# Kernel optimization log

Hardware: AMD Instinct MI355X
Metric: run time of the kernel (lower is better)

## Reference

```python
import jax, jax.numpy as jnp
import numpy as np

N = 200_000   # points
C = 20        # semantic classes
P = 256       # proposals (from bfs_cluster)
M = 400_000   # (proposal, point) pairs
CLUSTER_PROPOSE_POINTS = 100
VOXEL_SIZE = 0.02


def setup_inputs() -> dict:
    key = jax.random.key(0)
    k1, k2, k3, k4, k5 = jax.random.split(key, 5)
    return {
        "logit_pred": jax.random.normal(k1, (N, C), jnp.float32),
        "bias_pred": jax.random.normal(k2, (N, 3), jnp.float32),
        "coord": jax.random.normal(k3, (N, 3), jnp.float32) * 5.0,
        "proposal_ids": jax.random.randint(k4, (M,), 0, P, dtype=jnp.int32),
        "point_ids": jax.random.randint(k5, (M,), 0, N, dtype=jnp.int32),
    }


def reference(logit_pred, bias_pred, coord, proposal_ids, point_ids):
    # voxelized predicted instance centers (center_pred /= voxel_size)
    center_pred = (coord + bias_pred) / VOXEL_SIZE

    # softmax + argmax semantic prediction
    probs = jax.nn.softmax(logit_pred, axis=-1)          # [N, C]
    segment_pred = jnp.argmax(probs, axis=1)             # [N]

    # dense proposal mask construction (scatter): proposals_pred[pid, point] = 1
    proposals_pred = jnp.zeros((P, N), jnp.int32).at[proposal_ids, point_ids].set(1)
    counts = proposals_pred.sum(axis=1)                  # [P]
    proposals_mask = counts > CLUSTER_PROPOSE_POINTS     # [P] keep mask

    # instance class = semantic class of the representative (first) point per proposal
    rep = jax.ops.segment_min(point_ids, proposal_ids, num_segments=P)  # [P]
    instance_pred = segment_pred[jnp.clip(rep, 0, N - 1)]               # [P]

    # per-proposal mean confidence: mean over proposal points of probs[point, cls]
    conf = probs[:, instance_pred]                       # [N, P] gather of class columns
    score_sum = jnp.einsum("pn,np->p", proposals_pred.astype(probs.dtype), conf)
    pred_scores = jnp.where(proposals_mask,
                            score_sum / jnp.maximum(counts, 1).astype(probs.dtype),
                            0.0)                         # [P]

    # filtered masks/classes (kept at fixed shape; invalid rows zeroed / class -1)
    pred_masks = proposals_pred * proposals_mask[:, None].astype(jnp.int32)
    pred_classes = jnp.where(proposals_mask, instance_pred, -1)

    return pred_scores, pred_masks, pred_classes, bias_pred, probs
```

## Files before the change

kernel.cpp:

```cpp
#include <hip/hip_runtime.h>

static constexpr int    kN = 200000;
static constexpr int    kC = 20;
static constexpr int    kP = 256;
static constexpr int    kM = 400000;
static constexpr int    kThreshPts = 100;
static constexpr int    kRowCap = 2048;
static constexpr int    kLWords = kN / 32;
static constexpr int    kF4Total = kN * kC / 4;

typedef float nfloat4 __attribute__((ext_vector_type(4)));

static constexpr size_t OFF_SCORES  = 0;
static constexpr size_t OFF_MASKS   = 256;
static constexpr size_t OFF_CLASSES = OFF_MASKS + (size_t)kP * kN;
static constexpr size_t OFF_BIAS    = OFF_CLASSES + 256;
static constexpr size_t OFF_PROBS   = OFF_BIAS + 3 * (size_t)kN;

static constexpr size_t WS_CURSOR = 0;
static constexpr size_t WS_SEG    = 1024;
static constexpr size_t WS_ROWBUF = WS_SEG + (size_t)kN * 4;

__global__ void __launch_bounds__(256)
k_softmax(const float* __restrict__ logit,
          const float* __restrict__ bias,
          float* __restrict__ out,
          int* __restrict__ seg,
          int* __restrict__ cursor) {
    __shared__ float lds[256][21];
    int t = threadIdx.x;
    int gbase = blockIdx.x * 1280;

#pragma unroll
    for (int i = 0; i < 5; i++) {
        int g = gbase + i * 256 + t;
        if (g < kF4Total) {
            float4 v4 = ((const float4*)logit)[g];
            int lf = (g - gbase) * 4;
            float vv[4] = {v4.x, v4.y, v4.z, v4.w};
#pragma unroll
            for (int k = 0; k < 4; k++) {
                int fl = lf + k;
                lds[fl / kC][fl % kC] = vv[k];
            }
        }
    }
    if (blockIdx.x == 0) cursor[t] = 0;
    int tid = blockIdx.x * 256 + t;
    if (tid < 150000) {
        ((float4*)(out + OFF_BIAS))[tid] = ((const float4*)bias)[tid];
    }
    __syncthreads();

    bool valid = tid < kN;
    float v[kC];
    if (valid) {
#pragma unroll
        for (int i = 0; i < kC; i++) v[i] = lds[t][i];
        float m = v[0]; int arg = 0;
#pragma unroll
        for (int i = 1; i < kC; i++) if (v[i] > m) { m = v[i]; arg = i; }
        float ssum = 0.0f;
#pragma unroll
        for (int i = 0; i < kC; i++) { v[i] = __expf(v[i] - m); ssum += v[i]; }
        float inv = 1.0f / ssum;
#pragma unroll
        for (int i = 0; i < kC; i++) v[i] *= inv;
        seg[tid] = arg;
    }
    __syncthreads();
    if (valid) {
#pragma unroll
        for (int i = 0; i < kC; i++) lds[t][i] = v[i];
    }
    __syncthreads();

    float* probs = out + OFF_PROBS;
#pragma unroll
    for (int i = 0; i < 5; i++) {
        int g = gbase + i * 256 + t;
        if (g < kF4Total) {
            int lf = (g - gbase) * 4;
            float4 o;
            o.x = lds[(lf    ) / kC][(lf    ) % kC];
            o.y = lds[(lf + 1) / kC][(lf + 1) % kC];
            o.z = lds[(lf + 2) / kC][(lf + 2) % kC];
            o.w = lds[(lf + 3) / kC][(lf + 3) % kC];
            ((float4*)probs)[g] = o;
        }
    }
}

__global__ void k_bucket(const int* __restrict__ prop,
                         const int* __restrict__ pt,
                         int* __restrict__ cursor,
                         int* __restrict__ rowbuf) {
    __shared__ int s_cnt[kP];
    __shared__ int s_off[kP];
    int t = threadIdx.x;
    if (t < kP) s_cnt[t] = 0;
    __syncthreads();
    int base = blockIdx.x * 4096;
    int pv[4], nv[4], slot[4];
    bool val[4];
#pragma unroll
    for (int j = 0; j < 4; j++) {
        int idx = base + j * 1024 + t;
        val[j] = idx < kM;
        if (val[j]) {
            pv[j]   = prop[idx];
            nv[j]   = pt[idx];
            slot[j] = atomicAdd(&s_cnt[pv[j]], 1);
        }
    }
    __syncthreads();
    if (t < kP) s_off[t] = s_cnt[t] ? atomicAdd(&cursor[t], s_cnt[t]) : 0;
    __syncthreads();
#pragma unroll
    for (int j = 0; j < 4; j++) {
        if (val[j]) {
            int dst = s_off[pv[j]] + slot[j];
            if (dst < kRowCap) rowbuf[pv[j] * kRowCap + dst] = nv[j];
        }
    }
}

__global__ void __launch_bounds__(1024)
k_row(const int* __restrict__ rowbuf,
      const int* __restrict__ cursor,
      const int* __restrict__ seg,
      float* __restrict__ out) {
    __shared__ unsigned int lbits[kLWords];
    __shared__ int   s_redc[16];
    __shared__ int   s_redm[16];
    __shared__ float s_redf[16];
    __shared__ int   s_cls;
    __shared__ float s_fv;

    int p = blockIdx.x;
    int t = threadIdx.x;
    const float* probs = out + OFF_PROBS;

    for (int i = t; i < kLWords; i += 1024) lbits[i] = 0;
    int len = cursor[p];
    if (len > kRowCap) len = kRowCap;
    __syncthreads();

    int mymin = 0x7fffffff;
    const int* rb = rowbuf + p * kRowCap;
    for (int i = t; i < len; i += 1024) {
        int n = rb[i];
        atomicOr(&lbits[(unsigned)n >> 5], 1u << (n & 31));
        mymin = n < mymin ? n : mymin;
    }
    __syncthreads();

    int cnt = 0;
    for (int i = t; i < kLWords; i += 1024) cnt += __popc(lbits[i]);
    for (int off = 32; off; off >>= 1) {
        cnt += __shfl_down(cnt, off);
        int om = __shfl_down(mymin, off);
        mymin = om < mymin ? om : mymin;
    }
    if ((t & 63) == 0) { s_redc[t >> 6] = cnt; s_redm[t >> 6] = mymin; }
    __syncthreads();
    if (t == 0) {
        int tot = 0, mn = 0x7fffffff;
        for (int i = 0; i < 16; i++) {
            tot += s_redc[i];
            mn = s_redm[i] < mn ? s_redm[i] : mn;
        }
        int r = mn < 0 ? 0 : (mn > kN - 1 ? kN - 1 : mn);
        int c = seg[r];
        bool fl = tot > kThreshPts;
        s_cls = c;
        s_fv  = fl ? 1.0f : 0.0f;
        s_redc[0] = tot;
        out[OFF_CLASSES + p] = fl ? (float)c : -1.0f;
    }
    __syncthreads();
    int   tot = s_redc[0];
    float fv  = s_fv;
    int   c   = s_cls;

    float s = 0.0f;
    for (int i = t; i < len; i += 1024) {
        int n = rb[i];
        unsigned int bit = 1u << (n & 31);
        unsigned int old = atomicAnd(&lbits[(unsigned)n >> 5], ~bit);
        if (old & bit) s += probs[(size_t)n * kC + c];
    }
    for (int off = 32; off; off >>= 1) s += __shfl_down(s, off);
    if ((t & 63) == 0) s_redf[t >> 6] = s;
    __syncthreads();
    if (t == 0) {
        float stot = 0.0f;
        for (int i = 0; i < 16; i++) stot += s_redf[i];
        float denom = (float)(tot > 1 ? tot : 1);
        out[OFF_SCORES + p] = (fv != 0.0f) ? stot / denom : 0.0f;
    }

    for (int i = t; i < len; i += 1024) {
        int n = rb[i];
        atomicOr(&lbits[(unsigned)n >> 5], 1u << (n & 31));
    }
    __syncthreads();

    nfloat4* mrow = (nfloat4*)(out + OFF_MASKS) + (size_t)p * (kN / 4);
    for (int f = t; f < kN / 4; f += 1024) {
        unsigned int word = lbits[f >> 3];
        unsigned int b    = (word >> (((unsigned)f & 7u) * 4u)) & 0xFu;
        nfloat4 o;
        o.x = (b & 1u) ? fv : 0.0f;
        o.y = (b & 2u) ? fv : 0.0f;
        o.z = (b & 4u) ? fv : 0.0f;
        o.w = (b & 8u) ? fv : 0.0f;
        __builtin_nontemporal_store(o, &mrow[f]);
    }
}

extern "C" void kernel_launch(void* const* d_in, const int* in_sizes, int n_in,
                              void* d_out, int out_size, void* d_ws, size_t ws_size,
                              hipStream_t stream) {
    const float* logit = (const float*)d_in[0];
    const float* bias  = (const float*)d_in[1];
    const int* prop = (const int*)d_in[3];
    const int* pt   = (const int*)d_in[4];
    float* out = (float*)d_out;
    char*  ws  = (char*)d_ws;

    int* cursor = (int*)(ws + WS_CURSOR);
    int* seg    = (int*)(ws + WS_SEG);
    int* rowbuf = (int*)(ws + WS_ROWBUF);

    k_softmax<<<(kN + 255) / 256, 256, 0, stream>>>(logit, bias, out, seg, cursor);
    k_bucket<<<(kM + 4095) / 4096, 1024, 0, stream>>>(prop, pt, cursor, rowbuf);
    k_row<<<kP, 1024, 0, stream>>>(rowbuf, cursor, seg, out);
}
```

Before: 264.9 us.

## Split mask expansion into separate wide kernel reading global bitsets

Per-proposal bitsets built in LDS are now written to a global workspace. A new kernel with 4096 blocks of 256 threads expands them into the dense float mask output, replacing the loop inside the 256-block row kernel. Nontemporal stores become plain stores. The aim is to spread the roughly 200 MB mask write across many more blocks and waves than 256 large LDS-heavy blocks allow. The cost is an extra launch and a small global bitset round trip.

Result: no change. 266.3 us (+0.5%).

```diff
diff --git a/kernel.cpp b/kernel.cpp
--- a/kernel.cpp
+++ b/kernel.cpp
@@ -8,8 +8,8 @@
 static constexpr int    kRowCap = 2048;
 static constexpr int    kLWords = kN / 32;
 static constexpr int    kF4Total = kN * kC / 4;
-
-typedef float nfloat4 __attribute__((ext_vector_type(4)));
+static constexpr int    kSlices = 16;
+static constexpr int    kF4PerSlice = kN / 4 / kSlices;
 
 static constexpr size_t OFF_SCORES  = 0;
 static constexpr size_t OFF_MASKS   = 256;
@@ -18,8 +18,10 @@
 static constexpr size_t OFF_PROBS   = OFF_BIAS + 3 * (size_t)kN;
 
 static constexpr size_t WS_CURSOR = 0;
-static constexpr size_t WS_SEG    = 1024;
+static constexpr size_t WS_ROWVAL = 1024;
+static constexpr size_t WS_SEG    = 2048;
 static constexpr size_t WS_ROWBUF = WS_SEG + (size_t)kN * 4;
+static constexpr size_t WS_GBITS  = WS_ROWBUF + (size_t)kP * kRowCap * 4;
 
 __global__ void __launch_bounds__(256)
 k_softmax(const float* __restrict__ logit,
@@ -126,10 +128,12 @@
 }
 
 __global__ void __launch_bounds__(1024)
-k_row(const int* __restrict__ rowbuf,
-      const int* __restrict__ cursor,
-      const int* __restrict__ seg,
-      float* __restrict__ out) {
+k_meta(const int* __restrict__ rowbuf,
+       const int* __restrict__ cursor,
+       const int* __restrict__ seg,
+       unsigned int* __restrict__ gbits,
+       float* __restrict__ rowval,
+       float* __restrict__ out) {
     __shared__ unsigned int lbits[kLWords];
     __shared__ int   s_redc[16];
     __shared__ int   s_redm[16];
@@ -176,6 +180,7 @@
         s_cls = c;
         s_fv  = fl ? 1.0f : 0.0f;
         s_redc[0] = tot;
+        rowval[p] = fl ? 1.0f : 0.0f;
         out[OFF_CLASSES + p] = fl ? (float)c : -1.0f;
     }
     __syncthreads();
@@ -206,16 +211,30 @@
     }
     __syncthreads();
 
-    nfloat4* mrow = (nfloat4*)(out + OFF_MASKS) + (size_t)p * (kN / 4);
-    for (int f = t; f < kN / 4; f += 1024) {
-        unsigned int word = lbits[f >> 3];
+    unsigned int* grow = gbits + (size_t)p * kLWords;
+    for (int i = t; i < kLWords; i += 1024) grow[i] = lbits[i];
+}
+
+__global__ void __launch_bounds__(256)
+k_expand(const unsigned int* __restrict__ gbits,
+         const float* __restrict__ rowval,
+         float* __restrict__ masks) {
+    int p = blockIdx.x >> 4;
+    int q = blockIdx.x & 15;
+    float fv = rowval[p];
+    const unsigned int* row = gbits + (size_t)p * kLWords;
+    float4* mrow = (float4*)masks + (size_t)p * (kN / 4);
+    int fbase = q * kF4PerSlice;
+    int fend  = fbase + kF4PerSlice;
+    for (int f = fbase + threadIdx.x; f < fend; f += 256) {
+        unsigned int word = row[f >> 3];
         unsigned int b    = (word >> (((unsigned)f & 7u) * 4u)) & 0xFu;
-        nfloat4 o;
+        float4 o;
         o.x = (b & 1u) ? fv : 0.0f;
         o.y = (b & 2u) ? fv : 0.0f;
         o.z = (b & 4u) ? fv : 0.0f;
         o.w = (b & 8u) ? fv : 0.0f;
-        __builtin_nontemporal_store(o, &mrow[f]);
+        mrow[f] = o;
     }
 }
 
@@ -229,11 +248,14 @@
     float* out = (float*)d_out;
     char*  ws  = (char*)d_ws;
 
-    int* cursor = (int*)(ws + WS_CURSOR);
-    int* seg    = (int*)(ws + WS_SEG);
-    int* rowbuf = (int*)(ws + WS_ROWBUF);
+    int*          cursor = (int*)(ws + WS_CURSOR);
+    float*        rowval = (float*)(ws + WS_ROWVAL);
+    int*          seg    = (int*)(ws + WS_SEG);
+    int*          rowbuf = (int*)(ws + WS_ROWBUF);
+    unsigned int* gbits  = (unsigned int*)(ws + WS_GBITS);
 
     k_softmax<<<(kN + 255) / 256, 256, 0, stream>>>(logit, bias, out, seg, cursor);
     k_bucket<<<(kM + 4095) / 4096, 1024, 0, stream>>>(prop, pt, cursor, rowbuf);
-    k_row<<<kP, 1024, 0, stream>>>(rowbuf, cursor, seg, out);
-}
+    k_meta<<<kP, 1024, 0, stream>>>(rowbuf, cursor, seg, gbits, rowval, out);
+    k_expand<<<kP * kSlices, 256, 0, stream>>>(gbits, rowval, out + OFF_MASKS);
+}
```

## Split mask writing into bulk zero-fill and sparse scatter kernels

Applied to the files above, without the earlier changes.

Dense mask output is now produced by a separate grid-stride kernel that zero-fills the whole PxN mask region with plain float4 stores. A new scatter kernel then writes 1.0 only at the listed points of kept proposals, so the per-row metadata kernel no longer re-sets the bitmap or streams its row from LDS. The aim is a simpler, fully parallel bulk-fill over 1024 blocks instead of 256 large blocks doing bitmap decode. It adds two launches and random scattered stores, and drops the nontemporal store hint.

After: 263.0 us. Within noise of the previous version (-0.7%).

```diff
diff --git a/kernel.cpp b/kernel.cpp
--- a/kernel.cpp
+++ b/kernel.cpp
@@ -9,8 +9,6 @@
 static constexpr int    kLWords = kN / 32;
 static constexpr int    kF4Total = kN * kC / 4;
 
-typedef float nfloat4 __attribute__((ext_vector_type(4)));
-
 static constexpr size_t OFF_SCORES  = 0;
 static constexpr size_t OFF_MASKS   = 256;
 static constexpr size_t OFF_CLASSES = OFF_MASKS + (size_t)kP * kN;
@@ -18,8 +16,18 @@
 static constexpr size_t OFF_PROBS   = OFF_BIAS + 3 * (size_t)kN;
 
 static constexpr size_t WS_CURSOR = 0;
-static constexpr size_t WS_SEG    = 1024;
+static constexpr size_t WS_ROWVAL = 1024;
+static constexpr size_t WS_SEG    = 2048;
 static constexpr size_t WS_ROWBUF = WS_SEG + (size_t)kN * 4;
+
+__global__ void __launch_bounds__(256)
+k_zero(float4* __restrict__ masks) {
+    const size_t total = (size_t)kP * kN / 4;
+    size_t stride = (size_t)gridDim.x * 256;
+    float4 z = make_float4(0.0f, 0.0f, 0.0f, 0.0f);
+    for (size_t f = (size_t)blockIdx.x * 256 + threadIdx.x; f < total; f += stride)
+        masks[f] = z;
+}
 
 __global__ void __launch_bounds__(256)
 k_softmax(const float* __restrict__ logit,
@@ -126,10 +134,11 @@
 }
 
 __global__ void __launch_bounds__(1024)
-k_row(const int* __restrict__ rowbuf,
-      const int* __restrict__ cursor,
-      const int* __restrict__ seg,
-      float* __restrict__ out) {
+k_meta(const int* __restrict__ rowbuf,
+       const int* __restrict__ cursor,
+       const int* __restrict__ seg,
+       float* __restrict__ rowval,
+       float* __restrict__ out) {
     __shared__ unsigned int lbits[kLWords];
     __shared__ int   s_redc[16];
     __shared__ int   s_redm[16];
@@ -176,6 +185,7 @@
         s_cls = c;
         s_fv  = fl ? 1.0f : 0.0f;
         s_redc[0] = tot;
+        rowval[p] = fl ? 1.0f : 0.0f;
         out[OFF_CLASSES + p] = fl ? (float)c : -1.0f;
     }
     __syncthreads();
@@ -199,24 +209,22 @@
         float denom = (float)(tot > 1 ? tot : 1);
         out[OFF_SCORES + p] = (fv != 0.0f) ? stot / denom : 0.0f;
     }
-
-    for (int i = t; i < len; i += 1024) {
-        int n = rb[i];
-        atomicOr(&lbits[(unsigned)n >> 5], 1u << (n & 31));
-    }
-    __syncthreads();
-
-    nfloat4* mrow = (nfloat4*)(out + OFF_MASKS) + (size_t)p * (kN / 4);
-    for (int f = t; f < kN / 4; f += 1024) {
-        unsigned int word = lbits[f >> 3];
-        unsigned int b    = (word >> (((unsigned)f & 7u) * 4u)) & 0xFu;
-        nfloat4 o;
-        o.x = (b & 1u) ? fv : 0.0f;
-        o.y = (b & 2u) ? fv : 0.0f;
-        o.z = (b & 4u) ? fv : 0.0f;
-        o.w = (b & 8u) ? fv : 0.0f;
-        __builtin_nontemporal_store(o, &mrow[f]);
-    }
+}
+
+__global__ void __launch_bounds__(1024)
+k_set(const int* __restrict__ rowbuf,
+      const int* __restrict__ cursor,
+      const float* __restrict__ rowval,
+      float* __restrict__ masks) {
+    int p = blockIdx.x;
+    float fv = rowval[p];
+    if (fv == 0.0f) return;
+    int len = cursor[p];
+    if (len > kRowCap) len = kRowCap;
+    float* mrow = masks + (size_t)p * kN;
+    const int* rb = rowbuf + p * kRowCap;
+    for (int i = threadIdx.x; i < len; i += 1024)
+        mrow[rb[i]] = fv;
 }
 
 extern "C" void kernel_launch(void* const* d_in, const int* in_sizes, int n_in,
@@ -229,11 +237,14 @@
     float* out = (float*)d_out;
     char*  ws  = (char*)d_ws;
 
-    int* cursor = (int*)(ws + WS_CURSOR);
-    int* seg    = (int*)(ws + WS_SEG);
-    int* rowbuf = (int*)(ws + WS_ROWBUF);
-
+    int*   cursor = (int*)(ws + WS_CURSOR);
+    float* rowval = (float*)(ws + WS_ROWVAL);
+    int*   seg    = (int*)(ws + WS_SEG);
+    int*   rowbuf = (int*)(ws + WS_ROWBUF);
+
+    k_zero<<<1024, 256, 0, stream>>>((float4*)(out + OFF_MASKS));
     k_softmax<<<(kN + 255) / 256, 256, 0, stream>>>(logit, bias, out, seg, cursor);
     k_bucket<<<(kM + 4095) / 4096, 1024, 0, stream>>>(prop, pt, cursor, rowbuf);
-    k_row<<<kP, 1024, 0, stream>>>(rowbuf, cursor, seg, out);
-}
+    k_meta<<<kP, 1024, 0, stream>>>(rowbuf, cursor, seg, rowval, out);
+    k_set<<<kP, 1024, 0, stream>>>(rowbuf, cursor, rowval, out + OFF_MASKS);
+}
```
